# Kernel tuning notes

Measured on AMD Instinct MI355X. Metric: run time of the kernel, lower is better.

## Reference

```python
import jax, jax.numpy as jnp
import numpy as np

FP8_MAX = 448.0


def setup_inputs() -> dict:
    key = jax.random.key(0)
    kx, kw = jax.random.split(key)
    in_features, out_features = 1024, 1024
    x = jax.random.normal(kx, (32768, in_features), dtype=jnp.float32)
    # kaiming_uniform_ with a=sqrt(5): bound = sqrt(6/((1+a^2)*fan_in)) = sqrt(1/fan_in)
    bound = 1.0 / np.sqrt(in_features)
    weight = jax.random.uniform(kw, (out_features, in_features), dtype=jnp.float32,
                                minval=-bound, maxval=bound)
    bias = jnp.zeros((out_features,), dtype=jnp.float32)
    return {"x": x, "weight": weight, "bias": bias}


def reference(x, weight, bias):
    # per-tensor input quant
    input_scale = jnp.maximum(jnp.max(jnp.abs(x)) / FP8_MAX, 1e-12)
    x_q = jnp.round(jnp.clip(x / input_scale, -FP8_MAX, FP8_MAX))
    # per-output-channel weight quant
    weight_amax = jnp.max(jnp.abs(weight), axis=1)            # [out]
    weight_scale = jnp.maximum(weight_amax / FP8_MAX, 1e-12)  # [out]
    weight_q = jnp.round(jnp.clip(weight / weight_scale[:, None], -FP8_MAX, FP8_MAX))
    # integer-valued GEMM in fp32, then dequant + bias
    output_q = jnp.einsum('ti,oi->to', x_q, weight_q)          # [T, out]
    output = output_q * (input_scale * weight_scale)[None, :]
    return output + bias
```

## Files before the change

kernel.cpp:

```cpp
#include <hip/hip_runtime.h>
#include <hip/hip_fp16.h>

#define FP8_MAX 448.0f
#define M_ 32768
#define N_ 1024
#define K_ 1024
#define BM 128
#define BN 128
#define BK 64

typedef _Float16 f16x8 __attribute__((ext_vector_type(8)));
typedef _Float16 f16x4 __attribute__((ext_vector_type(4)));
typedef float f32x16 __attribute__((ext_vector_type(16)));

__device__ inline void gload_lds16(const void* g, void* l) {
    __builtin_amdgcn_global_load_lds(
        (const __attribute__((address_space(1))) void*)g,
        (__attribute__((address_space(3))) void*)l,
        16, 0, 0);
}

__global__ __launch_bounds__(256) void prep_kernel(const float* __restrict__ x,
                                                   const float* __restrict__ w,
                                                   float* __restrict__ xamax_part,
                                                   float* __restrict__ wscale,
                                                   _Float16* __restrict__ wq,
                                                   int n) {
    __shared__ float sm[4];
    if (blockIdx.x < 1024) {
        int row = blockIdx.x;
        const float4* wr4 = (const float4*)(w + (size_t)row * K_);
        float4 v = wr4[threadIdx.x];
        float m = fmaxf(fmaxf(fabsf(v.x), fabsf(v.y)), fmaxf(fabsf(v.z), fabsf(v.w)));
        #pragma unroll
        for (int off = 32; off > 0; off >>= 1)
            m = fmaxf(m, __shfl_down(m, off, 64));
        if ((threadIdx.x & 63) == 0) sm[threadIdx.x >> 6] = m;
        __syncthreads();
        m = fmaxf(fmaxf(sm[0], sm[1]), fmaxf(sm[2], sm[3]));
        float scale = fmaxf(m / FP8_MAX, 1e-12f);
        if (threadIdx.x == 0) wscale[row] = scale;
        float inv = 1.0f / scale;
        f16x4 o;
        o[0] = (_Float16)rintf(fminf(fmaxf(v.x * inv, -FP8_MAX), FP8_MAX));
        o[1] = (_Float16)rintf(fminf(fmaxf(v.y * inv, -FP8_MAX), FP8_MAX));
        o[2] = (_Float16)rintf(fminf(fmaxf(v.z * inv, -FP8_MAX), FP8_MAX));
        o[3] = (_Float16)rintf(fminf(fmaxf(v.w * inv, -FP8_MAX), FP8_MAX));
        ((f16x4*)(wq + (size_t)row * K_))[threadIdx.x] = o;
    } else {
        float m = 0.0f;
        const float4* x4 = (const float4*)x;
        int n4 = n >> 2;
        int stride = 2048 * 256;
        for (int i = (blockIdx.x - 1024) * 256 + threadIdx.x; i < n4; i += stride) {
            float4 v = x4[i];
            m = fmaxf(m, fmaxf(fmaxf(fabsf(v.x), fabsf(v.y)),
                               fmaxf(fabsf(v.z), fabsf(v.w))));
        }
        #pragma unroll
        for (int off = 32; off > 0; off >>= 1)
            m = fmaxf(m, __shfl_down(m, off, 64));
        if ((threadIdx.x & 63) == 0) sm[threadIdx.x >> 6] = m;
        __syncthreads();
        if (threadIdx.x == 0) {
            xamax_part[blockIdx.x - 1024] =
                fmaxf(fmaxf(sm[0], sm[1]), fmaxf(sm[2], sm[3]));
        }
    }
}

__global__ __launch_bounds__(256) void quant_x_kernel(const float* __restrict__ x,
                                                      const float* __restrict__ xamax_part,
                                                      float* __restrict__ xscale_out,
                                                      _Float16* __restrict__ xq,
                                                      int n) {
    __shared__ float sm[4];
    const float4* p4 = (const float4*)xamax_part;
    float4 a = p4[threadIdx.x];
    float4 b = p4[threadIdx.x + 256];
    float m = fmaxf(fmaxf(fmaxf(a.x, a.y), fmaxf(a.z, a.w)),
                    fmaxf(fmaxf(b.x, b.y), fmaxf(b.z, b.w)));
    #pragma unroll
    for (int off = 32; off > 0; off >>= 1)
        m = fmaxf(m, __shfl_down(m, off, 64));
    if ((threadIdx.x & 63) == 0) sm[threadIdx.x >> 6] = m;
    __syncthreads();
    float amax = fmaxf(fmaxf(sm[0], sm[1]), fmaxf(sm[2], sm[3]));
    float scale = fmaxf(amax / FP8_MAX, 1e-12f);
    if (threadIdx.x == 0) xscale_out[0] = scale;
    float inv = 1.0f / scale;

    const float4* x4 = (const float4*)x;
    f16x4* o4 = (f16x4*)xq;
    int n4 = n >> 2;
    int stride = gridDim.x * blockDim.x;
    for (int i = blockIdx.x * blockDim.x + threadIdx.x; i < n4; i += stride) {
        float4 v = x4[i];
        f16x4 o;
        o[0] = (_Float16)rintf(fminf(fmaxf(v.x * inv, -FP8_MAX), FP8_MAX));
        o[1] = (_Float16)rintf(fminf(fmaxf(v.y * inv, -FP8_MAX), FP8_MAX));
        o[2] = (_Float16)rintf(fminf(fmaxf(v.z * inv, -FP8_MAX), FP8_MAX));
        o[3] = (_Float16)rintf(fminf(fmaxf(v.w * inv, -FP8_MAX), FP8_MAX));
        o4[i] = o;
    }
}

__global__ __launch_bounds__(256) void gemm_kernel(const _Float16* __restrict__ xq,
                                                   const _Float16* __restrict__ wq,
                                                   const float* __restrict__ xscale,
                                                   const float* __restrict__ wscale,
                                                   const float* __restrict__ bias,
                                                   float* __restrict__ out) {
    __shared__ __align__(16) _Float16 sA[BM * BK];
    __shared__ __align__(16) _Float16 sB[BN * BK];

    const int tid  = threadIdx.x;
    const int wave = tid >> 6;
    const int lane = tid & 63;
    const int h   = lane >> 5;
    const int m32 = lane & 31;
    const int m7  = m32 & 7;
    const int wm = (wave >> 1) * 64;
    const int wn = (wave & 1) * 64;

    const int m0 = (int)(blockIdx.x & 255) * BM;
    const int n0 = (int)(blockIdx.x >> 8) * BN;

    const int trow = tid >> 3;
    const int tcol = (((tid & 7) ^ (trow & 7)) * 8);

    const _Float16* Ag = xq + ((size_t)(m0 + trow)) * K_ + tcol;
    const _Float16* Bg = wq + ((size_t)(n0 + trow)) * K_ + tcol;
    char* lA = (char*)sA + wave * 1024;
    char* lB = (char*)sB + wave * 1024;

    f32x16 acc[2][2] = {};

    for (int kt = 0; kt < K_; kt += BK) {
        #pragma unroll
        for (int rr = 0; rr < 4; ++rr) {
            gload_lds16(Ag + kt + (size_t)(rr * 32) * K_, lA + rr * 4096);
            gload_lds16(Bg + kt + (size_t)(rr * 32) * K_, lB + rr * 4096);
        }
        __syncthreads();
        #pragma unroll
        for (int ks = 0; ks < 4; ++ks) {
            f16x8 a[2], b[2];
            const int chunk = ks * 2 + h;
            const int pos = (chunk ^ m7) * 8;
            #pragma unroll
            for (int i = 0; i < 2; ++i)
                a[i] = *(const f16x8*)&sA[(wm + i * 32 + m32) * BK + pos];
            #pragma unroll
            for (int j = 0; j < 2; ++j)
                b[j] = *(const f16x8*)&sB[(wn + j * 32 + m32) * BK + pos];
            #pragma unroll
            for (int i = 0; i < 2; ++i)
                #pragma unroll
                for (int j = 0; j < 2; ++j)
                    acc[i][j] = __builtin_amdgcn_mfma_f32_32x32x16_f16(a[i], b[j], acc[i][j], 0, 0, 0);
        }
        __syncthreads();
    }

    float iscale = xscale[0];

    #pragma unroll
    for (int j = 0; j < 2; ++j) {
        int col = n0 + wn + j * 32 + m32;
        float sc = iscale * wscale[col];
        float bs = bias[col];
        #pragma unroll
        for (int i = 0; i < 2; ++i) {
            int rb = m0 + wm + i * 32 + 4 * h;
            #pragma unroll
            for (int reg = 0; reg < 16; ++reg) {
                int row = rb + (reg & 3) + 8 * (reg >> 2);
                out[(size_t)row * N_ + col] = acc[i][j][reg] * sc + bs;
            }
        }
    }
}

extern "C" void kernel_launch(void* const* d_in, const int* in_sizes, int n_in,
                              void* d_out, int out_size, void* d_ws, size_t ws_size,
                              hipStream_t stream) {
    const float* x    = (const float*)d_in[0];
    const float* w    = (const float*)d_in[1];
    const float* bias = (const float*)d_in[2];
    float* out = (float*)d_out;

    char* ws = (char*)d_ws;
    float* xscale      = (float*)ws;
    float* xamax_part  = (float*)(ws + 1024);
    float* wscale      = (float*)(ws + 16384);
    _Float16* wq       = (_Float16*)(ws + 32768);
    _Float16* xq       = (_Float16*)(ws + (4u << 20));

    prep_kernel<<<3072, 256, 0, stream>>>(x, w, xamax_part, wscale, wq, M_ * K_);
    quant_x_kernel<<<8192, 256, 0, stream>>>(x, xamax_part, xscale, xq, M_ * K_);
    gemm_kernel<<<2048, 256, 0, stream>>>(xq, wq, xscale, wscale, bias, out);
}
```

Before: 339.1 us.

## Fuse activation quantization into GEMM A-tile loading

Drops the separate x-quantization kernel and its fp16 intermediate buffer. The GEMM now finishes the amax reduction itself, then loads fp32 x tiles into registers, scales and rounds them, packs them to fp16 and stores them to LDS. This removes a full pass that wrote and re-read the quantized activations and one kernel launch. In exchange, each of the eight column tiles re-reads fp32 x, twice the bytes of the old fp16 copy, and the A tile now goes through registers with synchronous loads instead of the async global-to-LDS path.

New measurement: 368.2 us. +8.6%, slower.

```diff
diff --git a/kernel.cpp b/kernel.cpp
--- a/kernel.cpp
+++ b/kernel.cpp
@@ -11,6 +11,7 @@
 
 typedef _Float16 f16x8 __attribute__((ext_vector_type(8)));
 typedef _Float16 f16x4 __attribute__((ext_vector_type(4)));
+typedef __fp16  h16x2 __attribute__((ext_vector_type(2)));
 typedef float f32x16 __attribute__((ext_vector_type(16)));
 
 __device__ inline void gload_lds16(const void* g, void* l) {
@@ -69,52 +70,33 @@
     }
 }
 
-__global__ __launch_bounds__(256) void quant_x_kernel(const float* __restrict__ x,
-                                                      const float* __restrict__ xamax_part,
-                                                      float* __restrict__ xscale_out,
-                                                      _Float16* __restrict__ xq,
-                                                      int n) {
-    __shared__ float sm[4];
-    const float4* p4 = (const float4*)xamax_part;
-    float4 a = p4[threadIdx.x];
-    float4 b = p4[threadIdx.x + 256];
-    float m = fmaxf(fmaxf(fmaxf(a.x, a.y), fmaxf(a.z, a.w)),
-                    fmaxf(fmaxf(b.x, b.y), fmaxf(b.z, b.w)));
-    #pragma unroll
-    for (int off = 32; off > 0; off >>= 1)
-        m = fmaxf(m, __shfl_down(m, off, 64));
-    if ((threadIdx.x & 63) == 0) sm[threadIdx.x >> 6] = m;
-    __syncthreads();
-    float amax = fmaxf(fmaxf(sm[0], sm[1]), fmaxf(sm[2], sm[3]));
-    float scale = fmaxf(amax / FP8_MAX, 1e-12f);
-    if (threadIdx.x == 0) xscale_out[0] = scale;
-    float inv = 1.0f / scale;
-
-    const float4* x4 = (const float4*)x;
-    f16x4* o4 = (f16x4*)xq;
-    int n4 = n >> 2;
-    int stride = gridDim.x * blockDim.x;
-    for (int i = blockIdx.x * blockDim.x + threadIdx.x; i < n4; i += stride) {
-        float4 v = x4[i];
-        f16x4 o;
-        o[0] = (_Float16)rintf(fminf(fmaxf(v.x * inv, -FP8_MAX), FP8_MAX));
-        o[1] = (_Float16)rintf(fminf(fmaxf(v.y * inv, -FP8_MAX), FP8_MAX));
-        o[2] = (_Float16)rintf(fminf(fmaxf(v.z * inv, -FP8_MAX), FP8_MAX));
-        o[3] = (_Float16)rintf(fminf(fmaxf(v.w * inv, -FP8_MAX), FP8_MAX));
-        o4[i] = o;
-    }
-}
-
-__global__ __launch_bounds__(256) void gemm_kernel(const _Float16* __restrict__ xq,
+__global__ __launch_bounds__(256) void gemm_kernel(const float* __restrict__ x,
                                                    const _Float16* __restrict__ wq,
-                                                   const float* __restrict__ xscale,
+                                                   const float* __restrict__ xamax_part,
                                                    const float* __restrict__ wscale,
                                                    const float* __restrict__ bias,
                                                    float* __restrict__ out) {
     __shared__ __align__(16) _Float16 sA[BM * BK];
     __shared__ __align__(16) _Float16 sB[BN * BK];
 
-    const int tid  = threadIdx.x;
+    const int tid = threadIdx.x;
+
+    const float4* p4 = (const float4*)xamax_part;
+    float4 pa = p4[tid];
+    float4 pb = p4[tid + 256];
+    float m = fmaxf(fmaxf(fmaxf(pa.x, pa.y), fmaxf(pa.z, pa.w)),
+                    fmaxf(fmaxf(pb.x, pb.y), fmaxf(pb.z, pb.w)));
+    #pragma unroll
+    for (int off = 32; off > 0; off >>= 1)
+        m = fmaxf(m, __shfl_down(m, off, 64));
+    float* red = (float*)sA;
+    if ((tid & 63) == 0) red[tid >> 6] = m;
+    __syncthreads();
+    const float amax = fmaxf(fmaxf(red[0], red[1]), fmaxf(red[2], red[3]));
+    __syncthreads();
+    const float iscale = fmaxf(amax / FP8_MAX, 1e-12f);
+    const float inv = 1.0f / iscale;
+
     const int wave = tid >> 6;
     const int lane = tid & 63;
     const int h   = lane >> 5;
@@ -128,19 +110,35 @@
 
     const int trow = tid >> 3;
     const int tcol = (((tid & 7) ^ (trow & 7)) * 8);
+    const _Float16* Bg = wq + ((size_t)(n0 + trow)) * K_ + tcol;
+    char* lB = (char*)sB + wave * 1024;
 
-    const _Float16* Ag = xq + ((size_t)(m0 + trow)) * K_ + tcol;
-    const _Float16* Bg = wq + ((size_t)(n0 + trow)) * K_ + tcol;
-    char* lA = (char*)sA + wave * 1024;
-    char* lB = (char*)sB + wave * 1024;
+    const int arow = tid >> 3;
+    const int ach  = tid & 7;
+    const float* Ag = x + (size_t)(m0 + arow) * K_ + ach * 8;
+    _Float16* Aw = sA + (size_t)arow * BK + ((ach ^ (arow & 7)) * 8);
 
     f32x16 acc[2][2] = {};
 
     for (int kt = 0; kt < K_; kt += BK) {
         #pragma unroll
+        for (int rr = 0; rr < 4; ++rr)
+            gload_lds16(Bg + kt + (size_t)(rr * 32) * K_, lB + rr * 4096);
+        #pragma unroll
         for (int rr = 0; rr < 4; ++rr) {
-            gload_lds16(Ag + kt + (size_t)(rr * 32) * K_, lA + rr * 4096);
-            gload_lds16(Bg + kt + (size_t)(rr * 32) * K_, lB + rr * 4096);
+            const float* src = Ag + kt + (size_t)(rr * 32) * K_;
+            float4 v0 = *(const float4*)src;
+            float4 v1 = *(const float4*)(src + 4);
+            h16x2 t0 = __builtin_amdgcn_cvt_pkrtz(rintf(v0.x * inv), rintf(v0.y * inv));
+            h16x2 t1 = __builtin_amdgcn_cvt_pkrtz(rintf(v0.z * inv), rintf(v0.w * inv));
+            h16x2 t2 = __builtin_amdgcn_cvt_pkrtz(rintf(v1.x * inv), rintf(v1.y * inv));
+            h16x2 t3 = __builtin_amdgcn_cvt_pkrtz(rintf(v1.z * inv), rintf(v1.w * inv));
+            f16x8 q;
+            q[0] = (_Float16)t0[0]; q[1] = (_Float16)t0[1];
+            q[2] = (_Float16)t1[0]; q[3] = (_Float16)t1[1];
+            q[4] = (_Float16)t2[0]; q[5] = (_Float16)t2[1];
+            q[6] = (_Float16)t3[0]; q[7] = (_Float16)t3[1];
+            *(f16x8*)(Aw + (size_t)(rr * 32) * BK) = q;
         }
         __syncthreads();
         #pragma unroll
@@ -162,8 +160,6 @@
         }
         __syncthreads();
     }
-
-    float iscale = xscale[0];
 
     #pragma unroll
     for (int j = 0; j < 2; ++j) {
@@ -191,13 +187,10 @@
     float* out = (float*)d_out;
 
     char* ws = (char*)d_ws;
-    float* xscale      = (float*)ws;
     float* xamax_part  = (float*)(ws + 1024);
     float* wscale      = (float*)(ws + 16384);
     _Float16* wq       = (_Float16*)(ws + 32768);
-    _Float16* xq       = (_Float16*)(ws + (4u << 20));
 
     prep_kernel<<<3072, 256, 0, stream>>>(x, w, xamax_part, wscale, wq, M_ * K_);
-    quant_x_kernel<<<8192, 256, 0, stream>>>(x, xamax_part, xscale, xq, M_ * K_);
-    gemm_kernel<<<2048, 256, 0, stream>>>(xq, wq, xscale, wscale, bias, out);
+    gemm_kernel<<<2048, 256, 0, stream>>>(x, wq, xamax_part, wscale, bias, out);
 }
```
